# Kernel tuning notes

Measured on AMD Instinct MI355X. Metric: run time of the kernel, lower is better.

Reference implementation:

```python
import jax, jax.numpy as jnp
import numpy as np

B, N, M, D = 8, 2048, 2048, 9


def setup_inputs() -> dict:
    key = jax.random.key(0)
    k1, k2 = jax.random.split(key)
    outputs = jax.random.normal(k1, (B, N, D), dtype=jnp.float32)
    targets = jax.random.normal(k2, (B, M, D), dtype=jnp.float32)
    return {"outputs": outputs, "targets": targets, "k": 64}


def _pinv(A):
    # pinv(A) = (A^T A)^{-1} A^T, batched over leading dim (A: (B,D,D))
    AT = jnp.swapaxes(A, 1, 2)
    ATA = jnp.einsum('bij,bjk->bik', AT, A)
    return jnp.einsum('bij,bjk->bik', jnp.linalg.inv(ATA), AT)


def reference(outputs, targets, k):
    y_pred, y_true = outputs, targets  # (B,N,9), (B,M,9)
    mu = jnp.mean(y_true, axis=1, keepdims=True)          # (B,1,9)
    yc = y_true - mu                                       # (B,M,9)
    cov = jnp.einsum('bmd,bme->bde', yc, yc)               # (B,9,9)
    C = _pinv(cov)                                         # (B,9,9)

    # Original computes z = (y_true_i - y_pred_j) - mu, then z^T C z for all
    # (i,j) pairs. Expand the quadratic form to avoid the (B,M,N,9) tensor:
    #   z = a_i - b_j with a_i = y_true_i - mu, b_j = y_pred_j
    #   z^T C z = a^T C a + b^T C b - a^T (C + C^T) b
    a = yc                                                 # (B,M,9)
    b = y_pred                                             # (B,N,9)
    Csym = C + jnp.swapaxes(C, 1, 2)
    qa = jnp.einsum('bmd,bde,bme->bm', a, C, a)            # (B,M)
    qb = jnp.einsum('bnd,bde,bne->bn', b, C, b)            # (B,N)
    cross = jnp.einsum('bmd,bde,bne->bmn', a, Csym, b)     # (B,M,N)
    D_norm = qa[:, :, None] + qb[:, None, :] - cross       # (B,M,N)

    # topk over dim=1 (M axis): move M last, take largest k
    vals, _ = jax.lax.top_k(jnp.swapaxes(D_norm, 1, 2), k)  # (B,N,k)
    return jnp.mean(vals)
```

## Files before the change

kernel.cpp:

```cpp
#include <hip/hip_runtime.h>
#include <stdint.h>

constexpr int B_ = 8, N_ = 2048, M_ = 2048, K_ = 64;

constexpr int WS_QB   = 1024;
constexpr int WS_U9   = 18432;
constexpr int WS_PART = 182272;
constexpr int PL = 1024;
constexpr int CHUNK = 10 * PL;

__global__ __launch_bounds__(256) void stats_pinv_kernel(const float* __restrict__ outputs,
                                                         const float* __restrict__ targets,
                                                         float* __restrict__ ws)
{
    const int b = blockIdx.x, t = threadIdx.x;

    float s[9], cc[45];
#pragma unroll
    for (int d = 0; d < 9; ++d) s[d] = 0.f;
#pragma unroll
    for (int i = 0; i < 45; ++i) cc[i] = 0.f;

    const float* T = targets + (size_t)b * M_ * 9;
#pragma unroll
    for (int r = 0; r < 8; ++r) {
        const float* row = T + (r * 256 + t) * 9;
        float y[9];
#pragma unroll
        for (int d = 0; d < 9; ++d) { y[d] = row[d]; s[d] += y[d]; }
        int idx = 0;
#pragma unroll
        for (int i = 0; i < 9; ++i)
#pragma unroll
            for (int j = i; j < 9; ++j) { cc[idx] = fmaf(y[i], y[j], cc[idx]); ++idx; }
    }
#pragma unroll
    for (int o = 32; o; o >>= 1) {
#pragma unroll
        for (int d = 0; d < 9; ++d) s[d] += __shfl_xor(s[d], o, 64);
#pragma unroll
        for (int i = 0; i < 45; ++i) cc[i] += __shfl_xor(cc[i], o, 64);
    }
    __shared__ float red[4][54];
    __shared__ float smom[54];
    const int wave = t >> 6, lane = t & 63;
    if (lane == 0) {
#pragma unroll
        for (int d = 0; d < 9; ++d) red[wave][d] = s[d];
#pragma unroll
        for (int i = 0; i < 45; ++i) red[wave][9 + i] = cc[i];
    }
    __syncthreads();

    __shared__ double As[81], G[81], Inv[81], Cm[81], fcol[9], smu[9];
    __shared__ float sSf[81], sMuF[9];

    if (wave == 0) {
        if (t < 54) smom[t] = red[0][t] + red[1][t] + red[2][t] + red[3][t];
        if (t < 9) {
            const double m = (double)smom[t] / M_;
            smu[t] = m;
            sMuF[t] = (float)m;
        }
#pragma unroll
        for (int cc2 = 0; cc2 < 2; ++cc2) {
            const int c = lane + cc2 * 64;
            if (cc2 == 0 || lane < 17) {
                const int i = c / 9, j = c % 9;
                const int ii = i < j ? i : j, jj = i < j ? j : i;
                const int tri = ii * 9 - ii * (ii - 1) / 2 + (jj - ii);
                As[c] = (double)smom[9 + tri] - (double)M_ * smu[i] * smu[j];
            }
        }
#pragma unroll
        for (int cc2 = 0; cc2 < 2; ++cc2) {
            const int c = lane + cc2 * 64;
            if (cc2 == 0 || lane < 17) {
                const int i = c / 9, j = c % 9;
                double sv = 0.0;
#pragma unroll
                for (int k = 0; k < 9; ++k) sv += As[k * 9 + i] * As[k * 9 + j];
                G[c] = sv;
                Inv[c] = (i == j) ? 1.0 : 0.0;
            }
        }
#pragma unroll 1
        for (int col = 0; col < 9; ++col) {
            const double p = G[col * 9 + col];
            if (lane >= col * 9 && lane < col * 9 + 9) { G[lane] /= p; Inv[lane] /= p; }
            if (lane < 17) {
                const int c2 = lane + 64;
                if (c2 >= col * 9 && c2 < col * 9 + 9) { G[c2] /= p; Inv[c2] /= p; }
            }
            if (lane < 9 && lane != col) fcol[lane] = G[lane * 9 + col];
            {
                const int r = lane / 9, j = lane % 9;
                if (r != col) {
                    const double f = fcol[r];
                    G[lane]   -= f * G[col * 9 + j];
                    Inv[lane] -= f * Inv[col * 9 + j];
                }
            }
            if (lane < 17) {
                const int c2 = lane + 64;
                const int r = c2 / 9, j = c2 % 9;
                if (r != col) {
                    const double f = fcol[r];
                    G[c2]   -= f * G[col * 9 + j];
                    Inv[c2] -= f * Inv[col * 9 + j];
                }
            }
        }
#pragma unroll
        for (int cc2 = 0; cc2 < 2; ++cc2) {
            const int c = lane + cc2 * 64;
            if (cc2 == 0 || lane < 17) {
                const int i = c / 9, j = c % 9;
                double sv = 0.0;
#pragma unroll
                for (int k = 0; k < 9; ++k) sv += Inv[i * 9 + k] * As[j * 9 + k];
                Cm[c] = sv;
            }
        }
#pragma unroll
        for (int cc2 = 0; cc2 < 2; ++cc2) {
            const int c = lane + cc2 * 64;
            if (cc2 == 0 || lane < 17) {
                const int i = c / 9, j = c % 9;
                sSf[c] = (float)(Cm[i * 9 + j] + Cm[j * 9 + i]);
            }
        }
    }
    __syncthreads();

    for (int c = t; c < N_; c += 256) {
        const float* r = outputs + ((size_t)b * N_ + c) * 9;
        float bv[9];
#pragma unroll
        for (int d = 0; d < 9; ++d) bv[d] = r[d];
        float q = 0.f;
#pragma unroll
        for (int d = 0; d < 9; ++d) {
            float v = 0.f;
#pragma unroll
            for (int e = 0; e < 9; ++e) v = fmaf(sSf[d * 9 + e], bv[e], v);
            q = fmaf(v, bv[d], q);
        }
        ws[WS_QB + b * N_ + c] = 0.5f * q;
    }

    for (int m = t; m < M_; m += 256) {
        const int h = m >> 10, mm = m & 1023;
        const float* r = T + (size_t)m * 9;
        float a[9];
#pragma unroll
        for (int d = 0; d < 9; ++d) a[d] = r[d] - sMuF[d];
        float* base = ws + WS_U9 + (size_t)(b * 2 + h) * CHUNK;
        float qa = 0.f;
#pragma unroll
        for (int d = 0; d < 9; ++d) {
            float u = 0.f;
#pragma unroll
            for (int e = 0; e < 9; ++e) u = fmaf(sSf[d * 9 + e], a[e], u);
            base[d * PL + mm] = u;
            qa = fmaf(u, a[d], qa);
        }
        base[9 * PL + mm] = 0.5f * qa;
    }
}

__global__ __launch_bounds__(512) void topk_kernel(const float* __restrict__ outputs,
                                                   float* __restrict__ ws)
{
    __shared__ float sT[10 * PL];
    const int b = blockIdx.y;
    const int tid = threadIdx.x;
    const int wave = tid >> 6, lane = tid & 63;
    const int n = blockIdx.x * 8 + wave;

    const float* brow = outputs + ((size_t)b * N_ + n) * 9;
    float ba[9];
#pragma unroll
    for (int d = 0; d < 9; ++d) ba[d] = brow[d];

    unsigned ua[32];
#pragma unroll
    for (int h = 0; h < 2; ++h) {
        __syncthreads();
        const float4* src = (const float4*)(ws + WS_U9 + (size_t)(b * 2 + h) * CHUNK);
        float4* dst = (float4*)sT;
#pragma unroll
        for (int i = 0; i < 5; ++i) dst[i * 512 + tid] = src[i * 512 + tid];
        __syncthreads();

#pragma unroll
        for (int g = 0; g < 4; ++g) {
            const int r0 = g * 256 + lane * 4;
            const float4 qv = *(const float4*)(sT + 9 * PL + r0);
            float a0 = qv.x, a1 = qv.y, a2 = qv.z, a3 = qv.w;
#pragma unroll
            for (int d = 0; d < 9; ++d) {
                const float4 uv = *(const float4*)(sT + d * PL + r0);
                const float bd = ba[d];
                a0 = fmaf(-uv.x, bd, a0);
                a1 = fmaf(-uv.y, bd, a1);
                a2 = fmaf(-uv.z, bd, a2);
                a3 = fmaf(-uv.w, bd, a3);
            }
            const int k0 = h * 16 + g * 4;
            const unsigned x0 = __float_as_uint(a0), x1 = __float_as_uint(a1);
            const unsigned x2 = __float_as_uint(a2), x3 = __float_as_uint(a3);
            ua[k0 + 0] = (x0 & 0x80000000u) ? ~x0 : (x0 | 0x80000000u);
            ua[k0 + 1] = (x1 & 0x80000000u) ? ~x1 : (x1 | 0x80000000u);
            ua[k0 + 2] = (x2 & 0x80000000u) ? ~x2 : (x2 | 0x80000000u);
            ua[k0 + 3] = (x3 & 0x80000000u) ? ~x3 : (x3 | 0x80000000u);
        }
    }

    unsigned ca = 0x80000000u;
#pragma unroll 1
    for (int bit = 30; bit >= 8; --bit) {
        const unsigned ta = ca | (1u << bit);
        int cnt = 0;
#pragma unroll
        for (int j = 0; j < 32; ++j) cnt += __popcll(__ballot(ua[j] >= ta));
        if (cnt >= K_) ca = ta;
    }

    float sa = 0.f;
    int ga = 0;
#pragma unroll
    for (int j = 0; j < 32; ++j) {
        const unsigned va = ua[j];
        const bool pa = va > ca;
        if (pa) sa += __uint_as_float(va ^ 0x80000000u);
        ga += __popcll(__ballot(pa));
    }
#pragma unroll
    for (int o = 32; o; o >>= 1) sa += __shfl_xor(sa, o, 64);

    __syncthreads();
    if (lane == 0) {
        const float tva = __uint_as_float(ca ^ 0x80000000u);
        const float qb = ws[WS_QB + b * N_ + n];
        sT[wave] = sa + (float)(K_ - ga) * tva + (float)K_ * qb;
    }
    __syncthreads();
    if (tid == 0) {
        float tsum = 0.f;
#pragma unroll
        for (int w = 0; w < 8; ++w) tsum += sT[w];
        ws[WS_PART + b * (N_ / 8) + blockIdx.x] = tsum;
    }
}

__global__ __launch_bounds__(256) void finalize_kernel(const float* __restrict__ ws,
                                                       float* __restrict__ out)
{
    const int tid = threadIdx.x;
    float s = 0.f;
#pragma unroll
    for (int i = 0; i < 8; ++i) s += ws[WS_PART + i * 256 + tid];
#pragma unroll
    for (int o = 32; o; o >>= 1) s += __shfl_xor(s, o, 64);
    __shared__ float r4[4];
    if ((tid & 63) == 0) r4[tid >> 6] = s;
    __syncthreads();
    if (tid == 0) out[0] = (r4[0] + r4[1] + r4[2] + r4[3]) * (1.0f / 1048576.0f);
}

extern "C" void kernel_launch(void* const* d_in, const int* in_sizes, int n_in,
                              void* d_out, int out_size, void* d_ws, size_t ws_size,
                              hipStream_t stream)
{
    (void)in_sizes; (void)n_in; (void)out_size; (void)ws_size;
    const float* outputs = (const float*)d_in[0];
    const float* targets = (const float*)d_in[1];
    float* ws  = (float*)d_ws;
    float* out = (float*)d_out;

    stats_pinv_kernel<<<B_, 256, 0, stream>>>(outputs, targets, ws);
    topk_kernel<<<dim3(N_ / 8, B_), 512, 0, stream>>>(outputs, ws);
    finalize_kernel<<<1, 256, 0, stream>>>(ws, out);
}
```

Before: 134.5 us.

## Double-buffer target chunks in LDS with register prefetch in topk kernel

```diff
diff --git a/kernel.cpp b/kernel.cpp
--- a/kernel.cpp
+++ b/kernel.cpp
@@ -6,8 +6,8 @@
 constexpr int WS_QB   = 1024;
 constexpr int WS_U9   = 18432;
 constexpr int WS_PART = 182272;
-constexpr int PL = 1024;
-constexpr int CHUNK = 10 * PL;
+constexpr int QPL = 512;
+constexpr int QCH = 10 * QPL;
 
 __global__ __launch_bounds__(256) void stats_pinv_kernel(const float* __restrict__ outputs,
                                                          const float* __restrict__ targets,
@@ -150,29 +150,29 @@
     }
 
     for (int m = t; m < M_; m += 256) {
-        const int h = m >> 10, mm = m & 1023;
+        const int q = m >> 9, mm = m & 511;
         const float* r = T + (size_t)m * 9;
         float a[9];
 #pragma unroll
         for (int d = 0; d < 9; ++d) a[d] = r[d] - sMuF[d];
-        float* base = ws + WS_U9 + (size_t)(b * 2 + h) * CHUNK;
+        float* base = ws + WS_U9 + (size_t)(b * 4 + q) * QCH;
         float qa = 0.f;
 #pragma unroll
         for (int d = 0; d < 9; ++d) {
             float u = 0.f;
 #pragma unroll
             for (int e = 0; e < 9; ++e) u = fmaf(sSf[d * 9 + e], a[e], u);
-            base[d * PL + mm] = u;
+            base[d * QPL + mm] = u;
             qa = fmaf(u, a[d], qa);
         }
-        base[9 * PL + mm] = 0.5f * qa;
+        base[9 * QPL + mm] = 0.5f * qa;
     }
 }
 
 __global__ __launch_bounds__(512) void topk_kernel(const float* __restrict__ outputs,
                                                    float* __restrict__ ws)
 {
-    __shared__ float sT[10 * PL];
+    __shared__ float sT[2][QCH];
     const int b = blockIdx.y;
     const int tid = threadIdx.x;
     const int wave = tid >> 6, lane = tid & 63;
@@ -183,31 +183,44 @@
 #pragma unroll
     for (int d = 0; d < 9; ++d) ba[d] = brow[d];
 
+    const float* ubase = ws + WS_U9 + (size_t)b * 4 * QCH;
+
+    {
+        const float2* src = (const float2*)ubase;
+        float2* dst = (float2*)sT[0];
+#pragma unroll
+        for (int i = 0; i < 5; ++i) dst[i * 512 + tid] = src[i * 512 + tid];
+    }
+    __syncthreads();
+
     unsigned ua[32];
 #pragma unroll
-    for (int h = 0; h < 2; ++h) {
-        __syncthreads();
-        const float4* src = (const float4*)(ws + WS_U9 + (size_t)(b * 2 + h) * CHUNK);
-        float4* dst = (float4*)sT;
-#pragma unroll
-        for (int i = 0; i < 5; ++i) dst[i * 512 + tid] = src[i * 512 + tid];
-        __syncthreads();
-
-#pragma unroll
-        for (int g = 0; g < 4; ++g) {
+    for (int q = 0; q < 4; ++q) {
+        float2 p0, p1, p2, p3, p4;
+        if (q < 3) {
+            const float2* src = (const float2*)(ubase + (size_t)(q + 1) * QCH);
+            p0 = src[0 * 512 + tid];
+            p1 = src[1 * 512 + tid];
+            p2 = src[2 * 512 + tid];
+            p3 = src[3 * 512 + tid];
+            p4 = src[4 * 512 + tid];
+        }
+        const float* cb = sT[q & 1];
+#pragma unroll
+        for (int g = 0; g < 2; ++g) {
             const int r0 = g * 256 + lane * 4;
-            const float4 qv = *(const float4*)(sT + 9 * PL + r0);
+            const float4 qv = *(const float4*)(cb + 9 * QPL + r0);
             float a0 = qv.x, a1 = qv.y, a2 = qv.z, a3 = qv.w;
 #pragma unroll
             for (int d = 0; d < 9; ++d) {
-                const float4 uv = *(const float4*)(sT + d * PL + r0);
+                const float4 uv = *(const float4*)(cb + d * QPL + r0);
                 const float bd = ba[d];
                 a0 = fmaf(-uv.x, bd, a0);
                 a1 = fmaf(-uv.y, bd, a1);
                 a2 = fmaf(-uv.z, bd, a2);
                 a3 = fmaf(-uv.w, bd, a3);
             }
-            const int k0 = h * 16 + g * 4;
+            const int k0 = q * 8 + g * 4;
             const unsigned x0 = __float_as_uint(a0), x1 = __float_as_uint(a1);
             const unsigned x2 = __float_as_uint(a2), x3 = __float_as_uint(a3);
             ua[k0 + 0] = (x0 & 0x80000000u) ? ~x0 : (x0 | 0x80000000u);
@@ -215,6 +228,15 @@
             ua[k0 + 2] = (x2 & 0x80000000u) ? ~x2 : (x2 | 0x80000000u);
             ua[k0 + 3] = (x3 & 0x80000000u) ? ~x3 : (x3 | 0x80000000u);
         }
+        if (q < 3) {
+            float2* dst = (float2*)sT[(q + 1) & 1];
+            dst[0 * 512 + tid] = p0;
+            dst[1 * 512 + tid] = p1;
+            dst[2 * 512 + tid] = p2;
+            dst[3 * 512 + tid] = p3;
+            dst[4 * 512 + tid] = p4;
+        }
+        __syncthreads();
     }
 
     unsigned ca = 0x80000000u;
@@ -239,17 +261,16 @@
 #pragma unroll
     for (int o = 32; o; o >>= 1) sa += __shfl_xor(sa, o, 64);
 
-    __syncthreads();
     if (lane == 0) {
         const float tva = __uint_as_float(ca ^ 0x80000000u);
         const float qb = ws[WS_QB + b * N_ + n];
-        sT[wave] = sa + (float)(K_ - ga) * tva + (float)K_ * qb;
+        sT[0][wave] = sa + (float)(K_ - ga) * tva + (float)K_ * qb;
     }
     __syncthreads();
     if (tid == 0) {
         float tsum = 0.f;
 #pragma unroll
-        for (int w = 0; w < 8; ++w) tsum += sT[w];
+        for (int w = 0; w < 8; ++w) tsum += sT[0][w];
         ws[WS_PART + b * (N_ / 8) + blockIdx.x] = tsum;
     }
 }
```

Result: slower. 144.6 us (+7.5%).
